# Optimization experiments

Hardware: AMD Instinct MI355X
Metric: run time of the kernel (lower is better)

Reference implementation:

```python
import jax, jax.numpy as jnp
import numpy as np
import math

N_EMBD = 1024
N_HEAD = 16
BLOCK_SIZE = 1024
B, T = 4, 1024


def setup_inputs() -> dict:
    key = jax.random.key(0)
    ks = jax.random.split(key, 7)
    C = N_EMBD
    # torch Linear weights stored here as [in, out] so y = x @ W + b
    return {
        "x": jax.random.normal(ks[0], (B, T, C), dtype=jnp.float32),
        "Wqk": jax.random.normal(ks[1], (C, 2 * C), dtype=jnp.float32) * 0.02,
        "bqk": jnp.zeros((2 * C,), dtype=jnp.float32),
        "Wgate": jax.random.normal(ks[2], (C, N_HEAD), dtype=jnp.float32) * 0.02,
        "bgate": jnp.zeros((N_HEAD,), dtype=jnp.float32),
        "Wproj": jax.random.normal(ks[3], (C, C), dtype=jnp.float32) * 0.02,
        "bproj": jnp.zeros((C,), dtype=jnp.float32),
    }


def reference(x, Wqk, bqk, Wgate, bgate, Wproj, bproj):
    Bx, Tx, C = x.shape
    H = N_HEAD
    D = C // H
    # per-head geometrically shrinking causal windows (static, from init args)
    windows = jnp.array([max(4, BLOCK_SIZE // (2 ** h)) for h in range(H)], dtype=jnp.int32)

    qk = x @ Wqk + bqk                      # [B,T,2C]
    q, k = jnp.split(qk, 2, axis=-1)
    v = k                                   # module sets v = k chunk

    # [B,H,T,D]
    q = q.reshape(Bx, Tx, H, D).transpose(0, 2, 1, 3)
    k = k.reshape(Bx, Tx, H, D).transpose(0, 2, 1, 3)
    v = v.reshape(Bx, Tx, H, D).transpose(0, 2, 1, 3)

    i = jnp.arange(Tx)[:, None]
    j = jnp.arange(Tx)[None, :]
    # mask[h,i,j] = causal AND within window: j in [i-window+1, i]
    mask = (j <= i)[None] & (j > i - windows[:, None, None])   # [H,T,T]

    att = jnp.einsum("bhtd,bhsd->bhts", q, k) * (1.0 / math.sqrt(D))
    att = jnp.where(mask[None], att, -jnp.inf)
    att = jax.nn.softmax(att, axis=-1)      # diagonal always unmasked -> safe

    out = jnp.einsum("bhts,bhsd->bhtd", att, v)   # [B,H,T,D]
    combined = out.transpose(0, 2, 1, 3)          # [B,T,H,D]

    gates = jax.nn.softmax(x @ Wgate + bgate, axis=-1)    # [B,T,H]
    gated = (combined * gates[..., None]).reshape(Bx, Tx, C)
    return gated @ Wproj + bproj
```

## Files before the change

kernel.cpp:

```cpp
#include <hip/hip_runtime.h>

typedef __attribute__((ext_vector_type(8))) short bf16x8;
typedef __attribute__((ext_vector_type(4))) float f32x4;

#define T_SEQ 1024
#define NH 16
#define CEMB 1024

__device__ __forceinline__ float asf(unsigned int u){ union{unsigned int i;float f;}x; x.i=u; return x.f; }
__device__ __forceinline__ float bf2f(unsigned short u){ return asf(((unsigned int)u)<<16); }
__device__ __forceinline__ unsigned short f2bf(float f){
  union{float f;unsigned int i;}x; x.f=f;
  unsigned int r = x.i + 0x7FFFu + ((x.i>>16)&1u);
  return (unsigned short)(r>>16);
}
__device__ __forceinline__ f32x4 MFMA16(bf16x8 a, bf16x8 b, f32x4 c){
  return __builtin_amdgcn_mfma_f32_16x16x32_bf16(a, b, c, 0,0,0);
}

__global__ void cvt_bf16_kernel(const float* __restrict__ in, unsigned short* __restrict__ out, int n){
  int i = (blockIdx.x*blockDim.x + threadIdx.x)*4;
  if (i >= n) return;
  float4 v = *reinterpret_cast<const float4*>(in + i);
  ushort4 o; o.x=f2bf(v.x); o.y=f2bf(v.y); o.z=f2bf(v.z); o.w=f2bf(v.w);
  *reinterpret_cast<ushort4*>(out + i) = o;
}

__global__ void gates_kernel(const float* __restrict__ x, const float* __restrict__ Wg,
                             const float* __restrict__ bg, float* __restrict__ gates){
  const int lane = threadIdx.x & 63;
  const int row  = blockIdx.x*4 + (threadIdx.x>>6);
  const float* xr = x + (size_t)row*CEMB;
  float acc[NH];
  #pragma unroll
  for (int h=0;h<NH;h++) acc[h]=0.f;
  for (int i=0;i<CEMB/64;i++){
    float xv = xr[i*64 + lane];
    const float4* wg = reinterpret_cast<const float4*>(Wg + (size_t)(i*64+lane)*NH);
    float4 a=wg[0], b=wg[1], c=wg[2], d=wg[3];
    acc[0]+=xv*a.x; acc[1]+=xv*a.y; acc[2]+=xv*a.z; acc[3]+=xv*a.w;
    acc[4]+=xv*b.x; acc[5]+=xv*b.y; acc[6]+=xv*b.z; acc[7]+=xv*b.w;
    acc[8]+=xv*c.x; acc[9]+=xv*c.y; acc[10]+=xv*c.z; acc[11]+=xv*c.w;
    acc[12]+=xv*d.x; acc[13]+=xv*d.y; acc[14]+=xv*d.z; acc[15]+=xv*d.w;
  }
  #pragma unroll
  for (int h=0;h<NH;h++){
    #pragma unroll
    for (int m=32;m;m>>=1) acc[h] += __shfl_xor(acc[h], m, 64);
  }
  float mx = -1e30f;
  #pragma unroll
  for (int h=0;h<NH;h++){ acc[h] += bg[h]; mx = fmaxf(mx, acc[h]); }
  float s = 0.f;
  #pragma unroll
  for (int h=0;h<NH;h++){ acc[h] = __expf(acc[h]-mx); s += acc[h]; }
  float g = 0.f;
  #pragma unroll
  for (int h=0;h<NH;h++) g = (lane==h) ? acc[h]/s : g;
  if (lane < NH) gates[(size_t)row*NH + lane] = g;
}

__global__ void wtrans_kernel(const float* __restrict__ Wqk, unsigned short* __restrict__ WqkT,
                              const float* __restrict__ Wproj, unsigned short* __restrict__ WprojT){
  __shared__ float tile[32][33];
  int blk = blockIdx.x;
  const float* W; unsigned short* Wt; int R, C, bx, by;
  if (blk < 2048){ W = Wqk;   Wt = WqkT;   R = 1024; C = 2048; bx = blk & 63; by = blk >> 6; }
  else { blk -= 2048; W = Wproj; Wt = WprojT; R = 1024; C = 1024; bx = blk & 31; by = blk >> 5; }
  const int c0 = bx*32, r0 = by*32;
  const int tx = threadIdx.x, ty = threadIdx.y;
  #pragma unroll
  for (int i=0;i<32;i+=8) tile[ty+i][tx] = W[(size_t)(r0+ty+i)*C + c0 + tx];
  __syncthreads();
  #pragma unroll
  for (int i=0;i<32;i+=8) Wt[(size_t)(c0+ty+i)*R + r0 + tx] = f2bf(tile[tx][ty+i]);
}

template<bool OUT_BF16, int BM>
__global__ __launch_bounds__(256)
void gemm_bt_kernel(const unsigned short* __restrict__ A, const unsigned short* __restrict__ Bt,
                    const float* __restrict__ bias, void* __restrict__ Cptr,
                    int M, int N, int K){
  constexpr int WCN   = (BM==128) ? 2 : 4;
  constexpr int MFRAG = 4;
  constexpr int NFRAG = 4/(WCN/2);
  constexpr int WCW   = 128/WCN;
  constexpr int AISS  = BM/32;
  __shared__ unsigned short lA0[BM*64], lA1[BM*64];
  __shared__ unsigned short lB0[128*64], lB1[128*64];
  const int tid = threadIdx.x;
  const int wid = tid>>6, lane = tid&63;
  const int nbm = M/BM;
  const int bid = blockIdx.x;
  const int bm = bid % nbm, bn = bid / nbm;
  const int wr = (BM==128) ? (wid>>1) : 0;
  const int wc = (BM==128) ? (wid&1) : wid;
  f32x4 acc[MFRAG][NFRAG] = {};

  const unsigned short* gA = A + (size_t)bm*BM*K;
  const unsigned short* gB = Bt + (size_t)bn*128*K;
  const int srow = lane>>3;
  const int schunk = lane&7;

#define GSTAGE(LA, LB, KK) do { \
  _Pragma("unroll") \
  for (int i_=0;i_<AISS;i_++){ \
    int rowi_ = (wid*AISS+i_)*8 + srow; \
    int cc_ = schunk ^ (rowi_ & 7); \
    __builtin_amdgcn_global_load_lds((const __attribute__((address_space(1))) void*)(gA + (size_t)rowi_*K + (KK) + cc_*8), \
        (__attribute__((address_space(3))) void*)&LA[(wid*AISS+i_)*512], 16, 0, 0); \
  } \
  _Pragma("unroll") \
  for (int i_=0;i_<4;i_++){ \
    int rowi_ = (wid*4+i_)*8 + srow; \
    int cc_ = schunk ^ (rowi_ & 7); \
    __builtin_amdgcn_global_load_lds((const __attribute__((address_space(1))) void*)(gB + (size_t)rowi_*K + (KK) + cc_*8), \
        (__attribute__((address_space(3))) void*)&LB[(wid*4+i_)*512], 16, 0, 0); \
  } \
} while(0)

#define GCOMPUTE(LA, LB) do { \
  _Pragma("unroll") \
  for (int ks_=0; ks_<2; ks_++){ \
    bf16x8 af_[MFRAG], bf_[NFRAG]; \
    _Pragma("unroll") \
    for (int m_=0;m_<MFRAG;m_++){ \
      int r_ = wr*64 + m_*16 + (lane&15); \
      int p_ = (ks_*4 + (lane>>4)) ^ (r_&7); \
      af_[m_] = *reinterpret_cast<const bf16x8*>(&LA[r_*64 + p_*8]); \
    } \
    _Pragma("unroll") \
    for (int n_=0;n_<NFRAG;n_++){ \
      int r_ = wc*WCW + n_*16 + (lane&15); \
      int p_ = (ks_*4 + (lane>>4)) ^ (r_&7); \
      bf_[n_] = *reinterpret_cast<const bf16x8*>(&LB[r_*64 + p_*8]); \
    } \
    _Pragma("unroll") \
    for (int m_=0;m_<MFRAG;m_++) \
      _Pragma("unroll") \
      for (int n_=0;n_<NFRAG;n_++) \
        acc[m_][n_] = __builtin_amdgcn_mfma_f32_16x16x32_bf16(af_[m_], bf_[n_], acc[m_][n_], 0,0,0); \
  } \
} while(0)

#define WAITL do { \
  if (BM==128) asm volatile("s_waitcnt vmcnt(8)" ::: "memory"); \
  else         asm volatile("s_waitcnt vmcnt(6)" ::: "memory"); \
  __builtin_amdgcn_s_barrier(); \
  __builtin_amdgcn_sched_barrier(0); \
} while(0)

  GSTAGE(lA0, lB0, 0);
  GSTAGE(lA1, lB1, 64);
  for (int k0=0; k0<K-128; k0+=128){
    WAITL;
    GCOMPUTE(lA0, lB0);
    __builtin_amdgcn_s_barrier();
    __builtin_amdgcn_sched_barrier(0);
    GSTAGE(lA0, lB0, k0+128);
    WAITL;
    GCOMPUTE(lA1, lB1);
    __builtin_amdgcn_s_barrier();
    __builtin_amdgcn_sched_barrier(0);
    GSTAGE(lA1, lB1, k0+192);
  }
  WAITL;
  GCOMPUTE(lA0, lB0);
  asm volatile("s_waitcnt vmcnt(0)" ::: "memory");
  __builtin_amdgcn_s_barrier();
  __builtin_amdgcn_sched_barrier(0);
  GCOMPUTE(lA1, lB1);
#undef GSTAGE
#undef GCOMPUTE
#undef WAITL

  const int rq = lane>>4;
  const int cl = lane&15;
  #pragma unroll
  for (int n=0;n<NFRAG;n++){
    int col = bn*128 + wc*WCW + n*16 + cl;
    float bv = bias[col];
    #pragma unroll
    for (int m=0;m<MFRAG;m++){
      int row = bm*BM + wr*64 + m*16 + rq*4;
      #pragma unroll
      for (int r=0;r<4;r++){
        float v = acc[m][n][r] + bv;
        if (OUT_BF16) ((unsigned short*)Cptr)[(size_t)(row+r)*N + col] = f2bf(v);
        else          ((float*)Cptr)[(size_t)(row+r)*N + col] = v;
      }
    }
  }
}

__global__ __launch_bounds__(256)
void kpack_kernel(const unsigned short* __restrict__ qk,
                  unsigned short* __restrict__ Kpack, unsigned short* __restrict__ Vpack){
  __shared__ unsigned short lT[64][68];
  const int blk = blockIdx.x;
  const int t0 = (blk & 15) * 64;
  const int bh = blk >> 4;
  const int b = bh >> 4, h = bh & 15;
  const int tid = threadIdx.x;
  #pragma unroll
  for (int it=0; it<2; it++){
    int idx = tid + it*256;
    int row = idx >> 3, c = idx & 7;
    uint4 v = *reinterpret_cast<const uint4*>(qk + ((size_t)(b*T_SEQ + t0 + row)*2048 + 1024 + h*64 + c*8));
    *reinterpret_cast<uint4*>(&lT[row][c*8]) = v;
  }
  __syncthreads();
  const int wid = tid>>6, lane = tid&63;
  const int g = lane>>4, li = lane&15;
  const int tile = wid>>1;
  const int kt = (t0>>5) + tile;
  #pragma unroll
  for (int ff=0; ff<2; ff++){
    const int f = (wid&1)*2 + ff;
    const int row = tile*32 + ((f>>1)<<4) + li;
    const int col = (f&1)*32 + g*8;
    uint4 v = *reinterpret_cast<const uint4*>(&lT[row][col]);
    *reinterpret_cast<uint4*>(Kpack + ((((size_t)bh*32 + kt)*4 + f)*64 + lane)*8) = v;
  }
  #pragma unroll
  for (int ff=0; ff<2; ff++){
    const int d4 = (wid&1)*2 + ff;
    unsigned short vv[8];
    #pragma unroll
    for (int j=0;j<8;j++) vv[j] = lT[tile*32 + g*8 + j][d4*16 + li];
    *reinterpret_cast<uint4*>(Vpack + ((((size_t)bh*32 + kt)*4 + d4)*64 + lane)*8) = *reinterpret_cast<const uint4*>(vv);
  }
}

__global__ __launch_bounds__(256)
void attn_mfma_kernel(const unsigned short* __restrict__ qk,
                      const unsigned short* __restrict__ Kpack,
                      const unsigned short* __restrict__ Vpack,
                      const float* __restrict__ gates, unsigned short* __restrict__ gated){
  __shared__ unsigned short lP[4][16*40];
  const int tid = threadIdx.x;
  const int wid = tid>>6, lane = tid&63;
  const int g = lane>>4, li = lane&15;

  const int V = wid*1024 + blockIdx.x;
  const int h = V>>8;
  const int rr = V&255;
  const int b = rr>>6, qw16 = rr&63;

  int w = 1024 >> h; if (w < 4) w = 4;
  const int qw0 = qw16*16;
  const int bh = b*NH + h;

  int mylo = qw0 - w + 1; if (mylo < 0) mylo = 0;
  const int kt_start = mylo >> 5;
  const int kt_end = (qw0 + 15) >> 5;

  const unsigned short* qbase = qk + ((size_t)(b*T_SEQ + qw0 + li)*2048 + h*64 + g*8);
  const bf16x8 aq0 = *reinterpret_cast<const bf16x8*>(qbase);
  const bf16x8 aq1 = *reinterpret_cast<const bf16x8*>(qbase + 32);

  f32x4 oacc[4] = {};
  float lsum[4] = {0.f,0.f,0.f,0.f};

  const unsigned short* kp = Kpack + (size_t)bh*32*4*512;
  const unsigned short* vp = Vpack + (size_t)bh*32*4*512;
  const int loff = lane*8;

  bf16x8 kf[4], kn[4], bv[4];
  #pragma unroll
  for (int f=0; f<4; f++)
    kf[f] = *reinterpret_cast<const bf16x8*>(kp + (kt_start*4 + f)*512 + loff);

  for (int kt = kt_start; kt <= kt_end; ++kt){
    #pragma unroll
    for (int d4=0; d4<4; d4++)
      bv[d4] = *reinterpret_cast<const bf16x8*>(vp + (kt*4 + d4)*512 + loff);
    {
      const int ktn = (kt < kt_end) ? kt+1 : kt_end;
      #pragma unroll
      for (int f=0; f<4; f++)
        kn[f] = *reinterpret_cast<const bf16x8*>(kp + (ktn*4 + f)*512 + loff);
    }

    f32x4 s0 = {}, s1 = {};
    s0 = MFMA16(aq0, kf[0], s0);
    s0 = MFMA16(aq1, kf[1], s0);
    s1 = MFMA16(aq0, kf[2], s1);
    s1 = MFMA16(aq1, kf[3], s1);

    const int k0 = kt*32;
    #pragma unroll
    for (int r=0;r<4;r++){
      const int t = qw0 + g*4 + r;
      const int ka = k0 + li;
      const int kb2 = ka + 16;
      const bool v0 = (ka <= t) && (ka > t - w);
      const bool v1 = (kb2 <= t) && (kb2 > t - w);
      const float p0 = v0 ? __expf(s0[r]*0.125f) : 0.f;
      const float p1 = v1 ? __expf(s1[r]*0.125f) : 0.f;
      lsum[r] += p0 + p1;
      const int q = g*4 + r;
      lP[wid][q*40 + li]      = f2bf(p0);
      lP[wid][q*40 + 16 + li] = f2bf(p1);
    }
    const bf16x8 pa = *reinterpret_cast<const bf16x8*>(&lP[wid][li*40 + g*8]);
    #pragma unroll
    for (int d4=0; d4<4; d4++)
      oacc[d4] = MFMA16(pa, bv[d4], oacc[d4]);
    #pragma unroll
    for (int i=0;i<4;i++) kf[i] = kn[i];
  }

  #pragma unroll
  for (int msk=1; msk<16; msk<<=1){
    #pragma unroll
    for (int r=0;r<4;r++) lsum[r] += __shfl_xor(lsum[r], msk, 64);
  }

  #pragma unroll
  for (int r=0;r<4;r++){
    const int t = qw0 + g*4 + r;
    const float gv = gates[(size_t)(b*T_SEQ + t)*NH + h];
    const float inv = gv / lsum[r];
    unsigned short* orow = gated + (size_t)(b*T_SEQ + t)*CEMB + h*64 + li;
    orow[0]  = f2bf(oacc[0][r]*inv);
    orow[16] = f2bf(oacc[1][r]*inv);
    orow[32] = f2bf(oacc[2][r]*inv);
    orow[48] = f2bf(oacc[3][r]*inv);
  }
}

extern "C" void kernel_launch(void* const* d_in, const int* in_sizes, int n_in,
                              void* d_out, int out_size, void* d_ws, size_t ws_size,
                              hipStream_t stream){
  const float* x     = (const float*)d_in[0];
  const float* Wqk   = (const float*)d_in[1];
  const float* bqk   = (const float*)d_in[2];
  const float* Wgate = (const float*)d_in[3];
  const float* bgate = (const float*)d_in[4];
  const float* Wproj = (const float*)d_in[5];
  const float* bproj = (const float*)d_in[6];
  float* out = (float*)d_out;

  unsigned short* x_bf   = (unsigned short*)d_ws;
  unsigned short* WqkT   = x_bf   + (size_t)4096*1024;
  unsigned short* WprojT = WqkT   + (size_t)2048*1024;
  unsigned short* qkb    = WprojT + (size_t)1024*1024;
  unsigned short* gated  = qkb    + (size_t)4096*2048;
  float*          gates  = (float*)(gated + (size_t)4096*1024);
  unsigned short* Kpack  = (unsigned short*)((char*)d_ws + (size_t)40*1024*1024);
  unsigned short* Vpack  = Kpack + (size_t)64*32*4*512;

  cvt_bf16_kernel<<<4096, 256, 0, stream>>>(x, x_bf, 4096*1024);
  wtrans_kernel<<<3072, dim3(32,8), 0, stream>>>(Wqk, WqkT, Wproj, WprojT);
  gates_kernel<<<1024, 256, 0, stream>>>(x, Wgate, bgate, gates);

  gemm_bt_kernel<true, 128><<<512, 256, 0, stream>>>(x_bf,  WqkT,   bqk,   qkb, 4096, 2048, 1024);
  kpack_kernel<<<1024, 256, 0, stream>>>(qkb, Kpack, Vpack);
  attn_mfma_kernel<<<1024, 256, 0, stream>>>(qkb, Kpack, Vpack, gates, gated);
  gemm_bt_kernel<false, 64><<<512, 256, 0, stream>>>(gated, WprojT, bproj, out, 4096, 1024, 1024);
}
```

Baseline: 101.4 us.

## Merge prep kernels into one launch and fuse K/V packing into QK GEMM epilogue

```diff
diff --git a/kernel.cpp b/kernel.cpp
--- a/kernel.cpp
+++ b/kernel.cpp
@@ -18,76 +18,83 @@
   return __builtin_amdgcn_mfma_f32_16x16x32_bf16(a, b, c, 0,0,0);
 }
 
-__global__ void cvt_bf16_kernel(const float* __restrict__ in, unsigned short* __restrict__ out, int n){
-  int i = (blockIdx.x*blockDim.x + threadIdx.x)*4;
-  if (i >= n) return;
-  float4 v = *reinterpret_cast<const float4*>(in + i);
-  ushort4 o; o.x=f2bf(v.x); o.y=f2bf(v.y); o.z=f2bf(v.z); o.w=f2bf(v.w);
-  *reinterpret_cast<ushort4*>(out + i) = o;
-}
-
-__global__ void gates_kernel(const float* __restrict__ x, const float* __restrict__ Wg,
-                             const float* __restrict__ bg, float* __restrict__ gates){
-  const int lane = threadIdx.x & 63;
-  const int row  = blockIdx.x*4 + (threadIdx.x>>6);
-  const float* xr = x + (size_t)row*CEMB;
-  float acc[NH];
-  #pragma unroll
-  for (int h=0;h<NH;h++) acc[h]=0.f;
-  for (int i=0;i<CEMB/64;i++){
-    float xv = xr[i*64 + lane];
-    const float4* wg = reinterpret_cast<const float4*>(Wg + (size_t)(i*64+lane)*NH);
-    float4 a=wg[0], b=wg[1], c=wg[2], d=wg[3];
-    acc[0]+=xv*a.x; acc[1]+=xv*a.y; acc[2]+=xv*a.z; acc[3]+=xv*a.w;
-    acc[4]+=xv*b.x; acc[5]+=xv*b.y; acc[6]+=xv*b.z; acc[7]+=xv*b.w;
-    acc[8]+=xv*c.x; acc[9]+=xv*c.y; acc[10]+=xv*c.z; acc[11]+=xv*c.w;
-    acc[12]+=xv*d.x; acc[13]+=xv*d.y; acc[14]+=xv*d.z; acc[15]+=xv*d.w;
-  }
-  #pragma unroll
-  for (int h=0;h<NH;h++){
-    #pragma unroll
-    for (int m=32;m;m>>=1) acc[h] += __shfl_xor(acc[h], m, 64);
-  }
-  float mx = -1e30f;
-  #pragma unroll
-  for (int h=0;h<NH;h++){ acc[h] += bg[h]; mx = fmaxf(mx, acc[h]); }
-  float s = 0.f;
-  #pragma unroll
-  for (int h=0;h<NH;h++){ acc[h] = __expf(acc[h]-mx); s += acc[h]; }
-  float g = 0.f;
-  #pragma unroll
-  for (int h=0;h<NH;h++) g = (lane==h) ? acc[h]/s : g;
-  if (lane < NH) gates[(size_t)row*NH + lane] = g;
-}
-
-__global__ void wtrans_kernel(const float* __restrict__ Wqk, unsigned short* __restrict__ WqkT,
-                              const float* __restrict__ Wproj, unsigned short* __restrict__ WprojT){
+__global__ __launch_bounds__(256)
+void prep_all_kernel(const float* __restrict__ x, unsigned short* __restrict__ x_bf,
+                     const float* __restrict__ Wqk, unsigned short* __restrict__ WqkT,
+                     const float* __restrict__ Wproj, unsigned short* __restrict__ WprojT,
+                     const float* __restrict__ Wg, const float* __restrict__ bg,
+                     float* __restrict__ gates){
   __shared__ float tile[32][33];
+  const int tid = threadIdx.x;
   int blk = blockIdx.x;
-  const float* W; unsigned short* Wt; int R, C, bx, by;
-  if (blk < 2048){ W = Wqk;   Wt = WqkT;   R = 1024; C = 2048; bx = blk & 63; by = blk >> 6; }
-  else { blk -= 2048; W = Wproj; Wt = WprojT; R = 1024; C = 1024; bx = blk & 31; by = blk >> 5; }
-  const int c0 = bx*32, r0 = by*32;
-  const int tx = threadIdx.x, ty = threadIdx.y;
-  #pragma unroll
-  for (int i=0;i<32;i+=8) tile[ty+i][tx] = W[(size_t)(r0+ty+i)*C + c0 + tx];
-  __syncthreads();
-  #pragma unroll
-  for (int i=0;i<32;i+=8) Wt[(size_t)(c0+ty+i)*R + r0 + tx] = f2bf(tile[tx][ty+i]);
-}
-
-template<bool OUT_BF16, int BM>
+  if (blk < 4096){
+    int i = (blk*256 + tid)*4;
+    float4 v = *reinterpret_cast<const float4*>(x + i);
+    ushort4 o; o.x=f2bf(v.x); o.y=f2bf(v.y); o.z=f2bf(v.z); o.w=f2bf(v.w);
+    *reinterpret_cast<ushort4*>(x_bf + i) = o;
+  } else if (blk < 7168){
+    blk -= 4096;
+    const float* W; unsigned short* Wt; int R, C, bx, by;
+    if (blk < 2048){ W = Wqk;   Wt = WqkT;   R = 1024; C = 2048; bx = blk & 63; by = blk >> 6; }
+    else { blk -= 2048; W = Wproj; Wt = WprojT; R = 1024; C = 1024; bx = blk & 31; by = blk >> 5; }
+    const int c0 = bx*32, r0 = by*32;
+    const int tx = tid & 31, ty = tid >> 5;
+    #pragma unroll
+    for (int i=0;i<32;i+=8) tile[ty+i][tx] = W[(size_t)(r0+ty+i)*C + c0 + tx];
+    __syncthreads();
+    #pragma unroll
+    for (int i=0;i<32;i+=8) Wt[(size_t)(c0+ty+i)*R + r0 + tx] = f2bf(tile[tx][ty+i]);
+  } else {
+    const int lane = tid & 63;
+    const int row  = (blk-7168)*4 + (tid>>6);
+    const float* xr = x + (size_t)row*CEMB;
+    float acc[NH];
+    #pragma unroll
+    for (int h=0;h<NH;h++) acc[h]=0.f;
+    for (int i=0;i<CEMB/64;i++){
+      float xv = xr[i*64 + lane];
+      const float4* wg = reinterpret_cast<const float4*>(Wg + (size_t)(i*64+lane)*NH);
+      float4 a=wg[0], b=wg[1], c=wg[2], d=wg[3];
+      acc[0]+=xv*a.x; acc[1]+=xv*a.y; acc[2]+=xv*a.z; acc[3]+=xv*a.w;
+      acc[4]+=xv*b.x; acc[5]+=xv*b.y; acc[6]+=xv*b.z; acc[7]+=xv*b.w;
+      acc[8]+=xv*c.x; acc[9]+=xv*c.y; acc[10]+=xv*c.z; acc[11]+=xv*c.w;
+      acc[12]+=xv*d.x; acc[13]+=xv*d.y; acc[14]+=xv*d.z; acc[15]+=xv*d.w;
+    }
+    #pragma unroll
+    for (int h=0;h<NH;h++){
+      #pragma unroll
+      for (int m=32;m;m>>=1) acc[h] += __shfl_xor(acc[h], m, 64);
+    }
+    float mx = -1e30f;
+    #pragma unroll
+    for (int h=0;h<NH;h++){ acc[h] += bg[h]; mx = fmaxf(mx, acc[h]); }
+    float s = 0.f;
+    #pragma unroll
+    for (int h=0;h<NH;h++){ acc[h] = __expf(acc[h]-mx); s += acc[h]; }
+    float g = 0.f;
+    #pragma unroll
+    for (int h=0;h<NH;h++) g = (lane==h) ? acc[h]/s : g;
+    if (lane < NH) gates[(size_t)row*NH + lane] = g;
+  }
+}
+
+template<bool OUT_BF16, int BM, bool PACK>
 __global__ __launch_bounds__(256)
 void gemm_bt_kernel(const unsigned short* __restrict__ A, const unsigned short* __restrict__ Bt,
                     const float* __restrict__ bias, void* __restrict__ Cptr,
-                    int M, int N, int K){
+                    int M, int N, int K,
+                    unsigned short* __restrict__ Kpack, unsigned short* __restrict__ Vpack){
   constexpr int WCN   = (BM==128) ? 2 : 4;
   constexpr int MFRAG = 4;
   constexpr int NFRAG = 4/(WCN/2);
   constexpr int WCW   = 128/WCN;
   constexpr int AISS  = BM/32;
-  __shared__ unsigned short lA0[BM*64], lA1[BM*64];
-  __shared__ unsigned short lB0[128*64], lB1[128*64];
+  constexpr int LDSN  = BM*64*2 + 128*64*2;
+  __shared__ __align__(16) unsigned short smem[LDSN];
+  unsigned short* lA0 = smem;
+  unsigned short* lA1 = smem + BM*64;
+  unsigned short* lB0 = smem + BM*64*2;
+  unsigned short* lB1 = smem + BM*64*2 + 128*64;
   const int tid = threadIdx.x;
   const int wid = tid>>6, lane = tid&63;
   const int nbm = M/BM;
@@ -176,6 +183,44 @@
 
   const int rq = lane>>4;
   const int cl = lane&15;
+
+  if (PACK && bn >= 8){
+    __syncthreads();
+    #pragma unroll
+    for (int n=0;n<NFRAG;n++){
+      const int c_l = wc*WCW + n*16 + cl;
+      const float bv = bias[bn*128 + c_l];
+      #pragma unroll
+      for (int m=0;m<MFRAG;m++){
+        const int r_l = wr*64 + m*16 + rq*4;
+        #pragma unroll
+        for (int r=0;r<4;r++)
+          smem[(r_l+r)*136 + c_l] = f2bf(acc[m][n][r] + bv);
+      }
+    }
+    __syncthreads();
+    const int b = bm>>3;
+    const int ktg0 = (bm&7)*4;
+    const int g = lane>>4, li = lane&15;
+    const int kt_l = wid;
+    #pragma unroll
+    for (int hh=0; hh<2; hh++){
+      const int bh = b*NH + (bn-8)*2 + hh;
+      const size_t fb = ((size_t)bh*32 + ktg0 + kt_l)*4;
+      #pragma unroll
+      for (int f=0; f<4; f++){
+        uint4 kv = *reinterpret_cast<const uint4*>(
+            &smem[(kt_l*32 + ((f>>1)<<4) + li)*136 + hh*64 + (f&1)*32 + g*8]);
+        *reinterpret_cast<uint4*>(Kpack + ((fb + f)*64 + lane)*8) = kv;
+        unsigned short vv[8];
+        #pragma unroll
+        for (int j=0;j<8;j++) vv[j] = smem[(kt_l*32 + g*8 + j)*136 + hh*64 + f*16 + li];
+        *reinterpret_cast<uint4*>(Vpack + ((fb + f)*64 + lane)*8) = *reinterpret_cast<const uint4*>(vv);
+      }
+    }
+    return;
+  }
+
   #pragma unroll
   for (int n=0;n<NFRAG;n++){
     int col = bn*128 + wc*WCW + n*16 + cl;
@@ -190,45 +235,6 @@
         else          ((float*)Cptr)[(size_t)(row+r)*N + col] = v;
       }
     }
-  }
-}
-
-__global__ __launch_bounds__(256)
-void kpack_kernel(const unsigned short* __restrict__ qk,
-                  unsigned short* __restrict__ Kpack, unsigned short* __restrict__ Vpack){
-  __shared__ unsigned short lT[64][68];
-  const int blk = blockIdx.x;
-  const int t0 = (blk & 15) * 64;
-  const int bh = blk >> 4;
-  const int b = bh >> 4, h = bh & 15;
-  const int tid = threadIdx.x;
-  #pragma unroll
-  for (int it=0; it<2; it++){
-    int idx = tid + it*256;
-    int row = idx >> 3, c = idx & 7;
-    uint4 v = *reinterpret_cast<const uint4*>(qk + ((size_t)(b*T_SEQ + t0 + row)*2048 + 1024 + h*64 + c*8));
-    *reinterpret_cast<uint4*>(&lT[row][c*8]) = v;
-  }
-  __syncthreads();
-  const int wid = tid>>6, lane = tid&63;
-  const int g = lane>>4, li = lane&15;
-  const int tile = wid>>1;
-  const int kt = (t0>>5) + tile;
-  #pragma unroll
-  for (int ff=0; ff<2; ff++){
-    const int f = (wid&1)*2 + ff;
-    const int row = tile*32 + ((f>>1)<<4) + li;
-    const int col = (f&1)*32 + g*8;
-    uint4 v = *reinterpret_cast<const uint4*>(&lT[row][col]);
-    *reinterpret_cast<uint4*>(Kpack + ((((size_t)bh*32 + kt)*4 + f)*64 + lane)*8) = v;
-  }
-  #pragma unroll
-  for (int ff=0; ff<2; ff++){
-    const int d4 = (wid&1)*2 + ff;
-    unsigned short vv[8];
-    #pragma unroll
-    for (int j=0;j<8;j++) vv[j] = lT[tile*32 + g*8 + j][d4*16 + li];
-    *reinterpret_cast<uint4*>(Vpack + ((((size_t)bh*32 + kt)*4 + d4)*64 + lane)*8) = *reinterpret_cast<const uint4*>(vv);
   }
 }
 
@@ -351,12 +357,11 @@
   unsigned short* Kpack  = (unsigned short*)((char*)d_ws + (size_t)40*1024*1024);
   unsigned short* Vpack  = Kpack + (size_t)64*32*4*512;
 
-  cvt_bf16_kernel<<<4096, 256, 0, stream>>>(x, x_bf, 4096*1024);
-  wtrans_kernel<<<3072, dim3(32,8), 0, stream>>>(Wqk, WqkT, Wproj, WprojT);
-  gates_kernel<<<1024, 256, 0, stream>>>(x, Wgate, bgate, gates);
-
-  gemm_bt_kernel<true, 128><<<512, 256, 0, stream>>>(x_bf,  WqkT,   bqk,   qkb, 4096, 2048, 1024);
-  kpack_kernel<<<1024, 256, 0, stream>>>(qkb, Kpack, Vpack);
+  prep_all_kernel<<<8192, 256, 0, stream>>>(x, x_bf, Wqk, WqkT, Wproj, WprojT, Wgate, bgate, gates);
+
+  gemm_bt_kernel<true, 128, true><<<512, 256, 0, stream>>>(x_bf, WqkT, bqk, qkb,
+                                                           4096, 2048, 1024, Kpack, Vpack);
   attn_mfma_kernel<<<1024, 256, 0, stream>>>(qkb, Kpack, Vpack, gates, gated);
-  gemm_bt_kernel<false, 64><<<512, 256, 0, stream>>>(gated, WprojT, bproj, out, 4096, 1024, 1024);
-}
+  gemm_bt_kernel<false, 64, false><<<512, 256, 0, stream>>>(gated, WprojT, bproj, out,
+                                                            4096, 1024, 1024, nullptr, nullptr);
+}
```

After: 97.99 us. 1.03x faster.
